# Kernel tuning notes

Hardware: AMD Instinct MI355X
Metric: run time of the kernel (lower is better)

Reference implementation:

```python
import jax, jax.numpy as jnp
import numpy as np

B, N, E = 2, 2048, 1024   # batch, seq_len, embed_dim (= hidden_dim)
H, HD = 16, 64            # num_heads, head_dim


def setup_inputs() -> dict:
    key = jax.random.key(0)
    ks = jax.random.split(key, 6)
    w = lambda k: jax.random.normal(k, (E, E), jnp.float32) * 0.02
    return {
        "x": jax.random.normal(ks[0], (B, N, E), jnp.float32),
        "Wq": w(ks[1]), "bq": jnp.zeros((E,), jnp.float32),
        "Wk": w(ks[2]), "bk": jnp.zeros((E,), jnp.float32),
        "Wv": w(ks[3]), "bv": jnp.zeros((E,), jnp.float32),
        "Wu": w(ks[4]), "bu": jnp.zeros((E,), jnp.float32),
        "Wo": w(ks[5]), "bo": jnp.zeros((E,), jnp.float32),
        "ln_g": jnp.ones((E,), jnp.float32),
        "ln_b": jnp.zeros((E,), jnp.float32),
    }


def reference(x, Wq, bq, Wk, bk, Wv, bv, Wu, bu, Wo, bo, ln_g, ln_b):
    # projections (torch Linear: x @ W.T + b)
    q = x @ Wq.T + bq
    k = x @ Wk.T + bk
    v = jax.nn.silu(x @ Wv.T + bv)   # uv_act = swish
    u = jax.nn.silu(x @ Wu.T + bu)
    # split heads: [B, N, H*HD] -> [B, H, N, HD]
    split = lambda t: t.reshape(B, N, H, HD).transpose(0, 2, 1, 3)
    q, k, v = split(q), split(k), split(v)
    # non-softmax attention: ReLU on scaled energy (no causal mask)
    energy = jnp.einsum("bhnd,bhmd->bhnm", q, k) / jnp.float32(np.sqrt(HD))
    energy = jax.nn.relu(energy)
    out = jnp.einsum("bhnm,bhmd->bhnd", energy, v)
    # merge heads: [B, H, N, HD] -> [B, N, H*HD]
    out = out.transpose(0, 2, 1, 3).reshape(B, N, H * HD)
    # layernorm over hidden_dim
    mu = out.mean(-1, keepdims=True)
    var = out.var(-1, keepdims=True)
    out = (out - mu) * jax.lax.rsqrt(var + 1e-5) * ln_g + ln_b
    # gate and output projection
    out = u * out
    return out @ Wo.T + bo
```

## Files before the change

### kernel.cpp

```cpp
#include <hip/hip_runtime.h>
#include <stdint.h>

typedef unsigned short u16;
typedef __attribute__((ext_vector_type(8))) short short8;
typedef __attribute__((ext_vector_type(4))) short short4v;
typedef __attribute__((ext_vector_type(4))) float floatx4;
typedef __attribute__((ext_vector_type(4))) int intx4;

#define B_ 2
#define N_ 2048
#define E_ 1024
#define H_ 16
#define HD_ 64
#define M_TOT (B_ * N_)

__device__ __forceinline__ float bf2f(u16 h) {
    union { unsigned u; float f; } c; c.u = ((unsigned)h) << 16; return c.f;
}
__device__ __forceinline__ u16 f2bf(float f) {
    union { float f; unsigned u; } c; c.f = f;
    unsigned r = c.u + 0x7FFFu + ((c.u >> 16) & 1u);
    return (u16)(r >> 16);
}
__device__ __forceinline__ float silu_f(float x) { return x / (1.f + __expf(-x)); }

template <typename T> __device__ __forceinline__ void store_out(T* p, float v);
template <> __device__ __forceinline__ void store_out<u16>(u16* p, float v)    { *p = f2bf(v); }
template <> __device__ __forceinline__ void store_out<float>(float* p, float v) { *p = v; }

__device__ __forceinline__ void gll16(const void* g, void* l) {
    __builtin_amdgcn_global_load_lds(
        (const __attribute__((address_space(1))) void*)g,
        (__attribute__((address_space(3))) void*)l,
        16, 0, 0);
}

__device__ __forceinline__ short4v relu_pack(floatx4 s) {
    union { float f; unsigned u; } c0, c1, c2, c3;
    c0.f = fmaxf(s[0], 0.f); c1.f = fmaxf(s[1], 0.f);
    c2.f = fmaxf(s[2], 0.f); c3.f = fmaxf(s[3], 0.f);
    unsigned lo = __builtin_amdgcn_perm(c1.u + 0x8000u, c0.u + 0x8000u, 0x07060302);
    unsigned hi = __builtin_amdgcn_perm(c3.u + 0x8000u, c2.u + 0x8000u, 0x07060302);
    union { unsigned v[2]; short4v s4; } r; r.v[0] = lo; r.v[1] = hi;
    return r.s4;
}

__launch_bounds__(256, 4)
__global__ void cvt6(const float* __restrict__ s0, const float* __restrict__ s1,
                     const float* __restrict__ s2, const float* __restrict__ s3,
                     const float* __restrict__ s4, const float* __restrict__ s5,
                     u16* __restrict__ d0, u16* __restrict__ d1,
                     u16* __restrict__ d2, u16* __restrict__ d3,
                     u16* __restrict__ d4, u16* __restrict__ d5)
{
    const int z = blockIdx.z;
    if (z > 0 && blockIdx.x >= E_ * E_ / 2048) return;
    const float* src = (z == 0) ? s0 : (z == 1) ? s1 : (z == 2) ? s2
                     : (z == 3) ? s3 : (z == 4) ? s4 : s5;
    u16* dst         = (z == 0) ? d0 : (z == 1) ? d1 : (z == 2) ? d2
                     : (z == 3) ? d3 : (z == 4) ? d4 : d5;
    const int i = (blockIdx.x * 256 + threadIdx.x) * 8;
    floatx4 a = *(const floatx4*)(src + i);
    floatx4 b = *(const floatx4*)(src + i + 4);
    union { u16 h[8]; intx4 v; } o;
    o.h[0] = f2bf(a[0]); o.h[1] = f2bf(a[1]); o.h[2] = f2bf(a[2]); o.h[3] = f2bf(a[3]);
    o.h[4] = f2bf(b[0]); o.h[5] = f2bf(b[1]); o.h[6] = f2bf(b[2]); o.h[7] = f2bf(b[3]);
    *(intx4*)(dst + i) = o.v;
}

template <typename OutT>
__launch_bounds__(256, 2)
__global__ void gemm4(const u16* __restrict__ A,
                      const u16* __restrict__ W0, const u16* __restrict__ W1,
                      const u16* __restrict__ W2, const u16* __restrict__ W3,
                      const float* __restrict__ bi0, const float* __restrict__ bi1,
                      const float* __restrict__ bi2, const float* __restrict__ bi3,
                      OutT* __restrict__ O0, OutT* __restrict__ O1,
                      OutT* __restrict__ O2, OutT* __restrict__ O3,
                      int actmask, int scalemask, int K)
{
    __shared__ u16 a_lds[128 * 32];
    __shared__ u16 b_lds[128 * 32];

    const int z = blockIdx.z;
    const u16* W    = (z == 0) ? W0 : (z == 1) ? W1 : (z == 2) ? W2 : W3;
    const float* Bi = (z == 0) ? bi0 : (z == 1) ? bi1 : (z == 2) ? bi2 : bi3;
    OutT* Out       = (z == 0) ? O0 : (z == 1) ? O1 : (z == 2) ? O2 : O3;
    const bool act = (actmask >> z) & 1;
    const float osc = ((scalemask >> z) & 1) ? 0.125f : 1.0f;

    const int t    = threadIdx.x;
    const int wave = t >> 6, lane = t & 63, quad = lane >> 4, l16 = lane & 15;
    const int wm = wave >> 1, wn = wave & 1;
    const int m0 = blockIdx.y * 128;
    const int n0 = blockIdx.x * 128;

    floatx4 acc[4][4];
    const floatx4 fz = {0.f, 0.f, 0.f, 0.f};
    for (int i = 0; i < 4; i++)
        for (int j = 0; j < 4; j++) acc[i][j] = fz;

    const int ar = t >> 2;
    const int ac = (t & 3) * 8;
    const u16* Ag0 = A + (size_t)(m0 + ar) * K + ac;
    const u16* Ag1 = A + (size_t)(m0 + 64 + ar) * K + ac;
    const u16* Bg0 = W + (size_t)(n0 + ar) * K + ac;
    const u16* Bg1 = W + (size_t)(n0 + 64 + ar) * K + ac;
    u16* al0 = a_lds + wave * 512;
    u16* al1 = a_lds + 2048 + wave * 512;
    u16* bl0 = b_lds + wave * 512;
    u16* bl1 = b_lds + 2048 + wave * 512;

    for (int k0 = 0; k0 < K; k0 += 32) {
        __syncthreads();
        gll16(Ag0 + k0, al0);
        gll16(Ag1 + k0, al1);
        gll16(Bg0 + k0, bl0);
        gll16(Bg1 + k0, bl1);
        __syncthreads();

        short8 af[4], bfr[4];
        for (int i = 0; i < 4; i++)
            af[i]  = *(const short8*)&a_lds[(wm * 64 + i * 16 + l16) * 32 + quad * 8];
        for (int j = 0; j < 4; j++)
            bfr[j] = *(const short8*)&b_lds[(wn * 64 + j * 16 + l16) * 32 + quad * 8];
        for (int i = 0; i < 4; i++)
            for (int j = 0; j < 4; j++)
                acc[i][j] = __builtin_amdgcn_mfma_f32_16x16x32_bf16(af[i], bfr[j], acc[i][j], 0, 0, 0);
    }

    float bias_v[4];
    for (int j = 0; j < 4; j++) bias_v[j] = Bi[n0 + wn * 64 + j * 16 + l16];

    for (int i = 0; i < 4; i++) {
        const int row = m0 + wm * 64 + i * 16 + quad * 4;
        for (int j = 0; j < 4; j++) {
            const int col = n0 + wn * 64 + j * 16 + l16;
            for (int r = 0; r < 4; r++) {
                float v = acc[i][j][r] + bias_v[j];
                if (act) v = silu_f(v);
                v *= osc;
                store_out<OutT>(&Out[(size_t)(row + r) * E_ + col], v);
            }
        }
    }
}

__launch_bounds__(256, 2)
__global__ void gemm_out(const u16* __restrict__ A, const u16* __restrict__ W,
                         const float* __restrict__ Bi, float* __restrict__ Out,
                         int K)
{
    __shared__ u16 a_lds[64 * 32];
    __shared__ u16 b_lds[128 * 32];

    const int t    = threadIdx.x;
    const int wave = t >> 6, lane = t & 63, quad = lane >> 4, l16 = lane & 15;
    const int m0 = blockIdx.y * 64;
    const int n0 = blockIdx.x * 128;

    floatx4 acc[4][2];
    const floatx4 fz = {0.f, 0.f, 0.f, 0.f};
    for (int i = 0; i < 4; i++)
        for (int j = 0; j < 2; j++) acc[i][j] = fz;

    const int ar = t >> 2;
    const int ac = (t & 3) * 8;
    const u16* Ag0 = A + (size_t)(m0 + ar) * K + ac;
    const u16* Bg0 = W + (size_t)(n0 + ar) * K + ac;
    const u16* Bg1 = W + (size_t)(n0 + 64 + ar) * K + ac;
    u16* al0 = a_lds + wave * 512;
    u16* bl0 = b_lds + wave * 512;
    u16* bl1 = b_lds + 2048 + wave * 512;

    for (int k0 = 0; k0 < K; k0 += 32) {
        __syncthreads();
        gll16(Ag0 + k0, al0);
        gll16(Bg0 + k0, bl0);
        gll16(Bg1 + k0, bl1);
        __syncthreads();

        short8 af[4], bfr[2];
        for (int i = 0; i < 4; i++)
            af[i]  = *(const short8*)&a_lds[(i * 16 + l16) * 32 + quad * 8];
        for (int j = 0; j < 2; j++)
            bfr[j] = *(const short8*)&b_lds[(wave * 32 + j * 16 + l16) * 32 + quad * 8];
        for (int i = 0; i < 4; i++)
            for (int j = 0; j < 2; j++)
                acc[i][j] = __builtin_amdgcn_mfma_f32_16x16x32_bf16(af[i], bfr[j], acc[i][j], 0, 0, 0);
    }

    float bias_v[2];
    for (int j = 0; j < 2; j++) bias_v[j] = Bi[n0 + wave * 32 + j * 16 + l16];

    for (int i = 0; i < 4; i++) {
        const int row = m0 + i * 16 + quad * 4;
        for (int j = 0; j < 2; j++) {
            const int col = n0 + wave * 32 + j * 16 + l16;
            for (int r = 0; r < 4; r++)
                Out[(size_t)(row + r) * E_ + col] = acc[i][j][r] + bias_v[j];
        }
    }
}

#define LK 72
#define LV 72
#define KSPLIT 2
#define KCHUNK (N_ / KSPLIT)

__launch_bounds__(256, 2)
__global__ void attn(const u16* __restrict__ Q, const u16* __restrict__ Kk,
                     const u16* __restrict__ V,
                     u16* __restrict__ P0, u16* __restrict__ P1)
{
    __shared__ u16 k_lds[64 * LK];
    __shared__ u16 v_lds[64 * LV];

    const int bh = blockIdx.y;
    const int b = bh >> 4, h = bh & 15;
    const int z = blockIdx.z;
    u16* __restrict__ Oa = (z == 0) ? P0 : P1;
    const int key_base = z * KCHUNK;

    const int t = threadIdx.x;
    const int wave = t >> 6, lane = t & 63, quad = lane >> 4, l16 = lane & 15;
    const int q0 = blockIdx.x * 256 + wave * 64;
    const size_t base = (size_t)b * N_ * E_ + h * HD_;

    short8 aq[4][2];
    for (int mi = 0; mi < 4; mi++)
        for (int ks = 0; ks < 2; ks++)
            aq[mi][ks] = *(const short8*)(Q + base + (size_t)(q0 + mi * 16 + l16) * E_ + ks * 32 + quad * 8);

    floatx4 o[4][4];
    const floatx4 fz = {0.f, 0.f, 0.f, 0.f};
    for (int mi = 0; mi < 4; mi++)
        for (int nd = 0; nd < 4; nd++) o[mi][nd] = fz;

    const int srow = t >> 2, sseg = (t & 3) * 16;
    const int prow = (srow & 32) + (((srow >> 2) & 1) << 4)
                   + (((srow >> 3) & 3) << 2) + (srow & 3);
    const u16* Ksrc = Kk + base + (size_t)(key_base + srow) * E_ + sseg;
    u16* kdst = &k_lds[prow * LK + sseg];

    const u16* Vsrc = V + base + (size_t)(key_base + srow) * E_ + sseg;

    for (int kt = 0; kt < KCHUNK / 64; kt++) {
        __syncthreads();
        const u16* kg = Ksrc + (size_t)(kt * 64) * E_;
        const u16* vg = Vsrc + (size_t)(kt * 64) * E_;
        intx4 kv0 = *(const intx4*)(kg);
        intx4 kv1 = *(const intx4*)(kg + 8);
        intx4 vv0 = *(const intx4*)(vg);
        intx4 vv1 = *(const intx4*)(vg + 8);
        *(intx4*)(kdst)     = kv0;
        *(intx4*)(kdst + 8) = kv1;
        const u16* v0p = (const u16*)&vv0;
        const u16* v1p = (const u16*)&vv1;
        for (int i = 0; i < 8; i++) {
            v_lds[(sseg + i) * LV + srow]     = v0p[i];
            v_lds[(sseg + 8 + i) * LV + srow] = v1p[i];
        }
        __syncthreads();

        for (int g = 0; g < 2; g++) {
            short8 ka[2][2];
            for (int tp = 0; tp < 2; tp++)
                for (int ks = 0; ks < 2; ks++)
                    ka[tp][ks] = *(const short8*)&k_lds[(g * 32 + tp * 16 + l16) * LK + ks * 32 + quad * 8];
            short8 bv[4];
            for (int nd = 0; nd < 4; nd++)
                bv[nd] = *(const short8*)&v_lds[(nd * 16 + l16) * LV + g * 32 + quad * 8];

            for (int mi = 0; mi < 4; mi++) {
                floatx4 c0 = __builtin_amdgcn_mfma_f32_16x16x32_bf16(ka[0][0], aq[mi][0], fz, 0, 0, 0);
                c0 = __builtin_amdgcn_mfma_f32_16x16x32_bf16(ka[0][1], aq[mi][1], c0, 0, 0, 0);
                floatx4 c1 = __builtin_amdgcn_mfma_f32_16x16x32_bf16(ka[1][0], aq[mi][0], fz, 0, 0, 0);
                c1 = __builtin_amdgcn_mfma_f32_16x16x32_bf16(ka[1][1], aq[mi][1], c1, 0, 0, 0);
                union { short4v h[2]; short8 s8; } sf;
                sf.h[0] = relu_pack(c0);
                sf.h[1] = relu_pack(c1);
                for (int nd = 0; nd < 4; nd++)
                    o[mi][nd] = __builtin_amdgcn_mfma_f32_16x16x32_bf16(sf.s8, bv[nd], o[mi][nd], 0, 0, 0);
            }
        }
    }

    for (int mi = 0; mi < 4; mi++)
        for (int nd = 0; nd < 4; nd++)
            for (int r = 0; r < 4; r++)
                Oa[(size_t)(b * N_ + q0 + mi * 16 + quad * 4 + r) * E_ + h * HD_ + nd * 16 + l16] =
                    f2bf(o[mi][nd][r]);
}

__launch_bounds__(256, 4)
__global__ void ln_gate(const u16* __restrict__ P0, const u16* __restrict__ P1,
                        const u16* __restrict__ U,
                        const float* __restrict__ G, const float* __restrict__ Bb,
                        u16* __restrict__ Out)
{
    const int row = blockIdx.x;
    const int t = threadIdx.x;
    const size_t idx = (size_t)row * E_ + t * 4;
    const short4v a0 = *(const short4v*)(P0 + idx);
    const short4v a1 = *(const short4v*)(P1 + idx);
    floatx4 v;
    for (int i = 0; i < 4; i++)
        v[i] = bf2f((u16)a0[i]) + bf2f((u16)a1[i]);
    float s  = v[0] + v[1] + v[2] + v[3];
    float ss = v[0] * v[0] + v[1] * v[1] + v[2] * v[2] + v[3] * v[3];
    for (int off = 32; off; off >>= 1) {
        s  += __shfl_down(s, off, 64);
        ss += __shfl_down(ss, off, 64);
    }
    __shared__ float red[8];
    const int wave = t >> 6, lane = t & 63;
    if (lane == 0) { red[wave] = s; red[4 + wave] = ss; }
    __syncthreads();
    const float S  = red[0] + red[1] + red[2] + red[3];
    const float SS = red[4] + red[5] + red[6] + red[7];
    const float mu  = S * (1.f / E_);
    const float var = SS * (1.f / E_) - mu * mu;
    const float rstd = rsqrtf(var + 1e-5f);

    short4v outv;
    for (int i = 0; i < 4; i++) {
        const int e = t * 4 + i;
        float y = (v[i] - mu) * rstd * G[e] + Bb[e];
        y *= bf2f(U[idx + i]);
        outv[i] = (short)f2bf(y);
    }
    *(short4v*)(Out + idx) = outv;
}

extern "C" void kernel_launch(void* const* d_in, const int* in_sizes, int n_in,
                              void* d_out, int out_size, void* d_ws, size_t ws_size,
                              hipStream_t stream)
{
    const float* x   = (const float*)d_in[0];
    const float* Wq  = (const float*)d_in[1];
    const float* bq  = (const float*)d_in[2];
    const float* Wk  = (const float*)d_in[3];
    const float* bk  = (const float*)d_in[4];
    const float* Wv  = (const float*)d_in[5];
    const float* bv  = (const float*)d_in[6];
    const float* Wu  = (const float*)d_in[7];
    const float* bu  = (const float*)d_in[8];
    const float* Wo  = (const float*)d_in[9];
    const float* bo  = (const float*)d_in[10];
    const float* lng = (const float*)d_in[11];
    const float* lnb = (const float*)d_in[12];

    char* ws = (char*)d_ws;
    u16*  qw  = (u16*)(ws);
    u16*  kw  = (u16*)(ws + 8388608);
    u16*  vw  = (u16*)(ws + 16777216);
    u16*  uw  = (u16*)(ws + 25165824);
    u16*  p0  = (u16*)(ws + 33554432);
    u16*  p1  = (u16*)(ws + 41943040);
    u16*  xb  = (u16*)(ws + 50331648);
    u16*  wbq = (u16*)(ws + 58720256);
    u16*  wbk = (u16*)(ws + 60817408);
    u16*  wbv = (u16*)(ws + 62914560);
    u16*  wbu = (u16*)(ws + 65011712);
    u16*  wbo = (u16*)(ws + 67108864);
    u16*  gw  = (u16*)(ws);

    float* out = (float*)d_out;

    const dim3 blk(256, 1, 1);

    cvt6<<<dim3(M_TOT * E_ / 2048, 1, 6), blk, 0, stream>>>(
        x, Wq, Wk, Wv, Wu, Wo, xb, wbq, wbk, wbv, wbu, wbo);
    gemm4<u16><<<dim3(8, 32, 4), blk, 0, stream>>>(xb, wbq, wbk, wbv, wbu,
                                                   bq, bk, bv, bu,
                                                   qw, kw, vw, uw, 0xC, 0x1, E_);
    attn<<<dim3(N_ / 256, B_ * H_, KSPLIT), blk, 0, stream>>>(qw, kw, vw, p0, p1);
    ln_gate<<<dim3(M_TOT, 1, 1), blk, 0, stream>>>(p0, p1, uw, lng, lnb, gw);
    gemm_out<<<dim3(E_ / 128, M_TOT / 64, 1), blk, 0, stream>>>(gw, wbo, bo, out, E_);
}
```

Measured before the change: 213.0 us.

## Replace QKVU projection GEMM with 256x256 double-buffered 8-wave pipelined kernel

```diff
diff --git a/kernel.cpp b/kernel.cpp
--- a/kernel.cpp
+++ b/kernel.cpp
@@ -23,10 +23,6 @@
     return (u16)(r >> 16);
 }
 __device__ __forceinline__ float silu_f(float x) { return x / (1.f + __expf(-x)); }
-
-template <typename T> __device__ __forceinline__ void store_out(T* p, float v);
-template <> __device__ __forceinline__ void store_out<u16>(u16* p, float v)    { *p = f2bf(v); }
-template <> __device__ __forceinline__ void store_out<float>(float* p, float v) { *p = v; }
 
 __device__ __forceinline__ void gll16(const void* g, void* l) {
     __builtin_amdgcn_global_load_lds(
@@ -68,79 +64,147 @@
     *(intx4*)(dst + i) = o.v;
 }
 
-template <typename OutT>
-__launch_bounds__(256, 2)
-__global__ void gemm4(const u16* __restrict__ A,
-                      const u16* __restrict__ W0, const u16* __restrict__ W1,
-                      const u16* __restrict__ W2, const u16* __restrict__ W3,
-                      const float* __restrict__ bi0, const float* __restrict__ bi1,
-                      const float* __restrict__ bi2, const float* __restrict__ bi3,
-                      OutT* __restrict__ O0, OutT* __restrict__ O1,
-                      OutT* __restrict__ O2, OutT* __restrict__ O3,
-                      int actmask, int scalemask, int K)
-{
-    __shared__ u16 a_lds[128 * 32];
-    __shared__ u16 b_lds[128 * 32];
+#define NTILES (E_ / 64)
+
+#define LDA_FRAGS(mlo, BUF)                                                        \
+    _Pragma("unroll")                                                              \
+    for (int mi = 0; mi < 4; mi++) {                                               \
+        af[(mlo) + mi][0] = *(const short8*)&lds[(BUF)*16384 + raA + ((mlo)+mi)*512];        \
+        af[(mlo) + mi][1] = *(const short8*)&lds[(BUF)*16384 + raA + 4096 + ((mlo)+mi)*512]; \
+    }
+
+#define LDB_FRAGS(blo, BUF)                                                        \
+    _Pragma("unroll")                                                              \
+    for (int bn = 0; bn < 2; bn++) {                                               \
+        bfr[bn][0] = *(const short8*)&lds[32768 + (BUF)*16384 + raB + ((blo)+bn)*512];        \
+        bfr[bn][1] = *(const short8*)&lds[32768 + (BUF)*16384 + raB + 4096 + ((blo)+bn)*512]; \
+    }
+
+#define MFMAQ(mlo, blo)                                                            \
+    _Pragma("unroll")                                                              \
+    for (int mi = 0; mi < 4; mi++)                                                 \
+        _Pragma("unroll")                                                          \
+        for (int bn = 0; bn < 2; bn++) {                                           \
+            acc[(mlo)+mi][(blo)+bn] = __builtin_amdgcn_mfma_f32_16x16x32_bf16(     \
+                af[(mlo)+mi][0], bfr[bn][0], acc[(mlo)+mi][(blo)+bn], 0, 0, 0);    \
+            acc[(mlo)+mi][(blo)+bn] = __builtin_amdgcn_mfma_f32_16x16x32_bf16(     \
+                af[(mlo)+mi][1], bfr[bn][1], acc[(mlo)+mi][(blo)+bn], 0, 0, 0);    \
+        }
+
+#define STAGE_AH(t2, h, BUFX)                                                      \
+    if ((t2) < NTILES) {                                                           \
+        gll16(As + (size_t)(h)*128*E_ + (t2)*64,      &lds[(BUFX)*16384 + (h)*8192 + wid*512]);        \
+        gll16(As + (size_t)(h)*128*E_ + (t2)*64 + 32, &lds[(BUFX)*16384 + (h)*8192 + 4096 + wid*512]); \
+    }
+
+#define STAGE_BH(t1, h, BUFX)                                                      \
+    if ((t1) < NTILES) {                                                           \
+        gll16(Bs + (size_t)(h)*128*E_ + (t1)*64,      &lds[32768 + (BUFX)*16384 + (h)*8192 + wid*512]);        \
+        gll16(Bs + (size_t)(h)*128*E_ + (t1)*64 + 32, &lds[32768 + (BUFX)*16384 + (h)*8192 + 4096 + wid*512]); \
+    }
+
+#define TILE(t, BUF) {                                                             \
+    LDA_FRAGS(0, BUF); LDB_FRAGS(0, BUF);                                          \
+    STAGE_BH((t)+1, 0, (BUF)^1);                                                   \
+    __builtin_amdgcn_s_barrier();                                                  \
+    __builtin_amdgcn_s_setprio(1); MFMAQ(0, 0); __builtin_amdgcn_s_setprio(0);     \
+    __builtin_amdgcn_s_barrier();                                                  \
+    LDA_FRAGS(4, BUF);                                                             \
+    STAGE_BH((t)+1, 1, (BUF)^1);                                                   \
+    __builtin_amdgcn_s_barrier();                                                  \
+    __builtin_amdgcn_s_setprio(1); MFMAQ(4, 0); __builtin_amdgcn_s_setprio(0);     \
+    __builtin_amdgcn_s_barrier();                                                  \
+    LDB_FRAGS(2, BUF);                                                             \
+    STAGE_AH((t)+2, 0, BUF);                                                       \
+    __builtin_amdgcn_s_barrier();                                                  \
+    __builtin_amdgcn_s_setprio(1); MFMAQ(4, 2); __builtin_amdgcn_s_setprio(0);     \
+    __builtin_amdgcn_s_barrier();                                                  \
+    STAGE_AH((t)+2, 1, BUF);                                                       \
+    __builtin_amdgcn_s_barrier();                                                  \
+    __builtin_amdgcn_s_setprio(1); MFMAQ(0, 2); __builtin_amdgcn_s_setprio(0);     \
+    asm volatile("s_waitcnt vmcnt(4)" ::: "memory");                               \
+    __builtin_amdgcn_s_barrier();                                                  \
+}
+
+__launch_bounds__(512, 2)
+__global__ void gemm8p(const u16* __restrict__ A,
+                       const u16* __restrict__ W0, const u16* __restrict__ W1,
+                       const u16* __restrict__ W2, const u16* __restrict__ W3,
+                       const float* __restrict__ bi0, const float* __restrict__ bi1,
+                       const float* __restrict__ bi2, const float* __restrict__ bi3,
+                       u16* __restrict__ O0, u16* __restrict__ O1,
+                       u16* __restrict__ O2, u16* __restrict__ O3,
+                       int actmask, int scalemask)
+{
+    __shared__ u16 lds[65536];
 
     const int z = blockIdx.z;
-    const u16* W    = (z == 0) ? W0 : (z == 1) ? W1 : (z == 2) ? W2 : W3;
+    const u16* Wp   = (z == 0) ? W0 : (z == 1) ? W1 : (z == 2) ? W2 : W3;
     const float* Bi = (z == 0) ? bi0 : (z == 1) ? bi1 : (z == 2) ? bi2 : bi3;
-    OutT* Out       = (z == 0) ? O0 : (z == 1) ? O1 : (z == 2) ? O2 : O3;
+    u16* Out        = (z == 0) ? O0 : (z == 1) ? O1 : (z == 2) ? O2 : O3;
     const bool act = (actmask >> z) & 1;
     const float osc = ((scalemask >> z) & 1) ? 0.125f : 1.0f;
 
-    const int t    = threadIdx.x;
-    const int wave = t >> 6, lane = t & 63, quad = lane >> 4, l16 = lane & 15;
-    const int wm = wave >> 1, wn = wave & 1;
-    const int m0 = blockIdx.y * 128;
-    const int n0 = blockIdx.x * 128;
-
-    floatx4 acc[4][4];
+    const int tid = threadIdx.x;
+    const int wid = tid >> 6, lane = tid & 63, quad = lane >> 4, l16 = lane & 15;
+    const int wm = wid >> 2, wn = wid & 3;
+    const int m0 = blockIdx.y * 256;
+    const int n0 = blockIdx.x * 256;
+
+    const int swz = ((l16 >> 3) & 1) * 16;
+    const int raA = wm * 8192 + l16 * 32 + ((quad * 8) ^ swz);
+    const int raB = (wn >> 1) * 8192 + ((wn & 1) * 64 + l16) * 32 + ((quad * 8) ^ swz);
+
+    const int srow_s = tid >> 2;
+    const int sce = ((tid & 3) * 8) ^ (((tid >> 5) & 1) * 16);
+    const u16* As = A  + (size_t)(m0 + srow_s) * E_ + sce;
+    const u16* Bs = Wp + (size_t)(n0 + srow_s) * E_ + sce;
+
+    floatx4 acc[8][4];
     const floatx4 fz = {0.f, 0.f, 0.f, 0.f};
-    for (int i = 0; i < 4; i++)
-        for (int j = 0; j < 4; j++) acc[i][j] = fz;
-
-    const int ar = t >> 2;
-    const int ac = (t & 3) * 8;
-    const u16* Ag0 = A + (size_t)(m0 + ar) * K + ac;
-    const u16* Ag1 = A + (size_t)(m0 + 64 + ar) * K + ac;
-    const u16* Bg0 = W + (size_t)(n0 + ar) * K + ac;
-    const u16* Bg1 = W + (size_t)(n0 + 64 + ar) * K + ac;
-    u16* al0 = a_lds + wave * 512;
-    u16* al1 = a_lds + 2048 + wave * 512;
-    u16* bl0 = b_lds + wave * 512;
-    u16* bl1 = b_lds + 2048 + wave * 512;
-
-    for (int k0 = 0; k0 < K; k0 += 32) {
-        __syncthreads();
-        gll16(Ag0 + k0, al0);
-        gll16(Ag1 + k0, al1);
-        gll16(Bg0 + k0, bl0);
-        gll16(Bg1 + k0, bl1);
-        __syncthreads();
-
-        short8 af[4], bfr[4];
-        for (int i = 0; i < 4; i++)
-            af[i]  = *(const short8*)&a_lds[(wm * 64 + i * 16 + l16) * 32 + quad * 8];
-        for (int j = 0; j < 4; j++)
-            bfr[j] = *(const short8*)&b_lds[(wn * 64 + j * 16 + l16) * 32 + quad * 8];
-        for (int i = 0; i < 4; i++)
-            for (int j = 0; j < 4; j++)
-                acc[i][j] = __builtin_amdgcn_mfma_f32_16x16x32_bf16(af[i], bfr[j], acc[i][j], 0, 0, 0);
+#pragma unroll
+    for (int mi = 0; mi < 8; mi++)
+#pragma unroll
+        for (int bn = 0; bn < 4; bn++) acc[mi][bn] = fz;
+
+    short8 af[8][2], bfr[2][2];
+
+    gll16(As,                  &lds[0     + wid*512]);
+    gll16(As + 32,             &lds[4096  + wid*512]);
+    gll16(As + 128*E_,         &lds[8192  + wid*512]);
+    gll16(As + 128*E_ + 32,    &lds[12288 + wid*512]);
+    gll16(Bs,                  &lds[32768 +  0    + wid*512]);
+    gll16(Bs + 32,             &lds[32768 + 4096  + wid*512]);
+    gll16(Bs + 128*E_,         &lds[32768 + 8192  + wid*512]);
+    gll16(Bs + 128*E_ + 32,    &lds[32768 + 12288 + wid*512]);
+    gll16(As + 64,             &lds[16384 +  0    + wid*512]);
+    gll16(As + 96,             &lds[16384 + 4096  + wid*512]);
+    gll16(As + 128*E_ + 64,    &lds[16384 + 8192  + wid*512]);
+    gll16(As + 128*E_ + 96,    &lds[16384 + 12288 + wid*512]);
+    asm volatile("s_waitcnt vmcnt(4)" ::: "memory");
+    __builtin_amdgcn_s_barrier();
+
+    for (int tt = 0; tt < NTILES; tt += 2) {
+        TILE(tt, 0);
+        TILE(tt + 1, 1);
     }
 
     float bias_v[4];
-    for (int j = 0; j < 4; j++) bias_v[j] = Bi[n0 + wn * 64 + j * 16 + l16];
-
-    for (int i = 0; i < 4; i++) {
-        const int row = m0 + wm * 64 + i * 16 + quad * 4;
-        for (int j = 0; j < 4; j++) {
-            const int col = n0 + wn * 64 + j * 16 + l16;
+#pragma unroll
+    for (int bn = 0; bn < 4; bn++) bias_v[bn] = Bi[n0 + wn * 64 + bn * 16 + l16];
+
+#pragma unroll
+    for (int mi = 0; mi < 8; mi++) {
+        const int row = m0 + wm * 128 + mi * 16 + quad * 4;
+#pragma unroll
+        for (int bn = 0; bn < 4; bn++) {
+            const int col = n0 + wn * 64 + bn * 16 + l16;
+#pragma unroll
             for (int r = 0; r < 4; r++) {
-                float v = acc[i][j][r] + bias_v[j];
+                float v = acc[mi][bn][r] + bias_v[bn];
                 if (act) v = silu_f(v);
                 v *= osc;
-                store_out<OutT>(&Out[(size_t)(row + r) * E_ + col], v);
+                Out[(size_t)(row + r) * E_ + col] = f2bf(v);
             }
         }
     }
@@ -242,7 +306,6 @@
                    + (((srow >> 3) & 3) << 2) + (srow & 3);
     const u16* Ksrc = Kk + base + (size_t)(key_base + srow) * E_ + sseg;
     u16* kdst = &k_lds[prow * LK + sseg];
-
     const u16* Vsrc = V + base + (size_t)(key_base + srow) * E_ + sseg;
 
     for (int kt = 0; kt < KCHUNK / 64; kt++) {
@@ -368,14 +431,11 @@
 
     float* out = (float*)d_out;
 
-    const dim3 blk(256, 1, 1);
-
-    cvt6<<<dim3(M_TOT * E_ / 2048, 1, 6), blk, 0, stream>>>(
+    cvt6<<<dim3(M_TOT * E_ / 2048, 1, 6), dim3(256, 1, 1), 0, stream>>>(
         x, Wq, Wk, Wv, Wu, Wo, xb, wbq, wbk, wbv, wbu, wbo);
-    gemm4<u16><<<dim3(8, 32, 4), blk, 0, stream>>>(xb, wbq, wbk, wbv, wbu,
-                                                   bq, bk, bv, bu,
-                                                   qw, kw, vw, uw, 0xC, 0x1, E_);
-    attn<<<dim3(N_ / 256, B_ * H_, KSPLIT), blk, 0, stream>>>(qw, kw, vw, p0, p1);
-    ln_gate<<<dim3(M_TOT, 1, 1), blk, 0, stream>>>(p0, p1, uw, lng, lnb, gw);
-    gemm_out<<<dim3(E_ / 128, M_TOT / 64, 1), blk, 0, stream>>>(gw, wbo, bo, out, E_);
-}
+    gemm8p<<<dim3(E_ / 256, M_TOT / 256, 4), dim3(512, 1, 1), 0, stream>>>(
+        xb, wbq, wbk, wbv, wbu, bq, bk, bv, bu, qw, kw, vw, uw, 0xC, 0x1);
+    attn<<<dim3(N_ / 256, B_ * H_, KSPLIT), dim3(256, 1, 1), 0, stream>>>(qw, kw, vw, p0, p1);
+    ln_gate<<<dim3(M_TOT, 1, 1), dim3(256, 1, 1), 0, stream>>>(p0, p1, uw, lng, lnb, gw);
+    gemm_out<<<dim3(E_ / 128, M_TOT / 64, 1), dim3(256, 1, 1), 0, stream>>>(gw, wbo, bo, out, E_);
+}
```

Result: no change. 210.1 us (-1.4%).

## Triple-buffer LDS loads in output GEMM with async prefetch pipeline

Applied to the files above, without the earlier changes.

```diff
diff --git a/kernel.cpp b/kernel.cpp
--- a/kernel.cpp
+++ b/kernel.cpp
@@ -151,8 +151,8 @@
                          const float* __restrict__ Bi, float* __restrict__ Out,
                          int K)
 {
-    __shared__ u16 a_lds[64 * 32];
-    __shared__ u16 b_lds[128 * 32];
+    __shared__ u16 a_lds[3][64 * 32];
+    __shared__ u16 b_lds[3][128 * 32];
 
     const int t    = threadIdx.x;
     const int wave = t >> 6, lane = t & 63, quad = lane >> 4, l16 = lane & 15;
@@ -169,26 +169,44 @@
     const u16* Ag0 = A + (size_t)(m0 + ar) * K + ac;
     const u16* Bg0 = W + (size_t)(n0 + ar) * K + ac;
     const u16* Bg1 = W + (size_t)(n0 + 64 + ar) * K + ac;
-    u16* al0 = a_lds + wave * 512;
-    u16* bl0 = b_lds + wave * 512;
-    u16* bl1 = b_lds + 2048 + wave * 512;
-
-    for (int k0 = 0; k0 < K; k0 += 32) {
-        __syncthreads();
-        gll16(Ag0 + k0, al0);
-        gll16(Bg0 + k0, bl0);
-        gll16(Bg1 + k0, bl1);
-        __syncthreads();
-
+
+    const int nt = K / 32;
+
+#define GO_STAGE(tt, bi) {                                      \
+        gll16(Ag0 + (tt) * 32, &a_lds[bi][wave * 512]);         \
+        gll16(Bg0 + (tt) * 32, &b_lds[bi][wave * 512]);         \
+        gll16(Bg1 + (tt) * 32, &b_lds[bi][2048 + wave * 512]); }
+
+    GO_STAGE(0, 0);
+    GO_STAGE(1, 1);
+    asm volatile("s_waitcnt vmcnt(3)" ::: "memory");
+    __builtin_amdgcn_s_barrier();
+
+    for (int tt = 0; tt < nt; tt++) {
+        const int bi = tt % 3;
+        if (tt + 2 < nt) {
+            GO_STAGE(tt + 2, (tt + 2) % 3);
+        }
         short8 af[4], bfr[2];
+#pragma unroll
         for (int i = 0; i < 4; i++)
-            af[i]  = *(const short8*)&a_lds[(i * 16 + l16) * 32 + quad * 8];
+            af[i]  = *(const short8*)&a_lds[bi][(i * 16 + l16) * 32 + quad * 8];
+#pragma unroll
         for (int j = 0; j < 2; j++)
-            bfr[j] = *(const short8*)&b_lds[(wave * 32 + j * 16 + l16) * 32 + quad * 8];
+            bfr[j] = *(const short8*)&b_lds[bi][(wave * 32 + j * 16 + l16) * 32 + quad * 8];
+#pragma unroll
         for (int i = 0; i < 4; i++)
+#pragma unroll
             for (int j = 0; j < 2; j++)
                 acc[i][j] = __builtin_amdgcn_mfma_f32_16x16x32_bf16(af[i], bfr[j], acc[i][j], 0, 0, 0);
-    }
+        if (tt + 2 < nt) {
+            asm volatile("s_waitcnt vmcnt(3)" ::: "memory");
+        } else {
+            asm volatile("s_waitcnt vmcnt(0)" ::: "memory");
+        }
+        __builtin_amdgcn_s_barrier();
+    }
+#undef GO_STAGE
 
     float bias_v[2];
     for (int j = 0; j < 2; j++) bias_v[j] = Bi[n0 + wave * 32 + j * 16 + l16];
@@ -242,7 +260,6 @@
                    + (((srow >> 3) & 3) << 2) + (srow & 3);
     const u16* Ksrc = Kk + base + (size_t)(key_base + srow) * E_ + sseg;
     u16* kdst = &k_lds[prow * LK + sseg];
-
     const u16* Vsrc = V + base + (size_t)(key_base + srow) * E_ + sseg;
 
     for (int kt = 0; kt < KCHUNK / 64; kt++) {
@@ -368,14 +385,11 @@
 
     float* out = (float*)d_out;
 
-    const dim3 blk(256, 1, 1);
-
-    cvt6<<<dim3(M_TOT * E_ / 2048, 1, 6), blk, 0, stream>>>(
+    cvt6<<<dim3(M_TOT * E_ / 2048, 1, 6), dim3(256, 1, 1), 0, stream>>>(
         x, Wq, Wk, Wv, Wu, Wo, xb, wbq, wbk, wbv, wbu, wbo);
-    gemm4<u16><<<dim3(8, 32, 4), blk, 0, stream>>>(xb, wbq, wbk, wbv, wbu,
-                                                   bq, bk, bv, bu,
-                                                   qw, kw, vw, uw, 0xC, 0x1, E_);
-    attn<<<dim3(N_ / 256, B_ * H_, KSPLIT), blk, 0, stream>>>(qw, kw, vw, p0, p1);
-    ln_gate<<<dim3(M_TOT, 1, 1), blk, 0, stream>>>(p0, p1, uw, lng, lnb, gw);
-    gemm_out<<<dim3(E_ / 128, M_TOT / 64, 1), blk, 0, stream>>>(gw, wbo, bo, out, E_);
-}
+    gemm4<u16><<<dim3(8, 32, 4), dim3(256, 1, 1), 0, stream>>>(
+        xb, wbq, wbk, wbv, wbu, bq, bk, bv, bu, qw, kw, vw, uw, 0xC, 0x1, E_);
+    attn<<<dim3(N_ / 256, B_ * H_, KSPLIT), dim3(256, 1, 1), 0, stream>>>(qw, kw, vw, p0, p1);
+    ln_gate<<<dim3(M_TOT, 1, 1), dim3(256, 1, 1), 0, stream>>>(p0, p1, uw, lng, lnb, gw);
+    gemm_out<<<dim3(E_ / 128, M_TOT / 64, 1), dim3(256, 1, 1), 0, stream>>>(gw, wbo, bo, out, E_);
+}
```

After: 216.0 us. Within noise of the previous version (+1.4%).
